# Performance work log

Measured on AMD Instinct MI355X. Metric: run time of the kernel, lower is better.

The kernel has to match this reference:

```python
import jax, jax.numpy as jnp
import numpy as np

B, N, C = 4, 4096, 64
K1, K2 = 4, 6
MLP1 = [128, 64, 64]
MLP2 = [128, 64]
EPS = 1e-5


def _sqdist(a, b):
    # a: [B,N,3], b: [B,M,3] -> [B,N,M]
    return (jnp.sum(a * a, -1)[:, :, None] + jnp.sum(b * b, -1)[:, None, :]
            - 2.0 * jnp.einsum('bnc,bmc->bnm', a, b))


def _knn_idx(k, xyz, new_xyz):
    # matches knn_point: topk of -square_distance(new_xyz, xyz)
    _, idx = jax.lax.top_k(-_sqdist(new_xyz, xyz), k)
    return idx  # [B,S,k]


def _gather(points, idx):
    # index_points: points [B,N,C], idx [B,S,K] -> [B,S,K,C]
    return jax.vmap(lambda p, i: p[i])(points, idx)


def _conv_bn_relu(x, w, g, b):
    # 1x1 Conv2d (no bias) + BatchNorm2d (train mode) + ReLU, channels-last
    y = jnp.einsum('bnkc,oc->bnko', x, w)
    m = jnp.mean(y, axis=(0, 1, 2), keepdims=True)
    v = jnp.var(y, axis=(0, 1, 2), keepdims=True)
    return jax.nn.relu((y - m) * jax.lax.rsqrt(v + EPS) * g + b)


def _quat_mul(a, b):
    # Hamilton product, matches mul_q_point ordering
    aw, ax, ay, az = a[..., 0], a[..., 1], a[..., 2], a[..., 3]
    bw, bx, by, bz = b[..., 0], b[..., 1], b[..., 2], b[..., 3]
    return jnp.stack([
        aw * bw - ax * bx - ay * by - az * bz,
        aw * bx + ax * bw + ay * bz - az * by,
        aw * by - ax * bz + ay * bw + az * bx,
        aw * bz + ax * by - ay * bx + az * bw], axis=-1)


def _inv_q(q):
    n2 = jnp.sum(q * q, -1, keepdims=True) + 1e-10
    return jnp.concatenate([q[..., :1], -q[..., 1:]], -1) / n2


def _qrot(q, v):
    # rotate points v [B,M,3] by quaternion q [B,4] via q * (0,v) * q^-1
    vq = jnp.concatenate([jnp.zeros(v.shape[:-1] + (1,), v.dtype), v], -1)
    qb = q[:, None, :]
    return _quat_mul(_quat_mul(qb, vq), _inv_q(q)[:, None, :])[..., 1:]


def setup_inputs() -> dict:
    key = jax.random.key(0)
    ks = jax.random.split(key, 32)

    def rn(i, shape, s=1.0):
        return jax.random.normal(ks[i], shape, jnp.float32) * s

    inp = {
        'pos1': rn(0, (B, N, 3)),
        'pos2': rn(1, (B, N, 3)),
        'feat1': rn(2, (B, N, C)),
        'feat2': rn(3, (B, N, C)),
        'q_coarse': rn(4, (B, 4)),
        't_coarse': rn(5, (B, 3)),
    }
    c1 = [2 * C + 3] + MLP1
    for i in range(len(MLP1)):
        inp['w1_%d' % i] = rn(6 + i, (c1[i + 1], c1[i]), 0.1)
        inp['g1_%d' % i] = jnp.ones((c1[i + 1],), jnp.float32)
        inp['b1_%d' % i] = jnp.zeros((c1[i + 1],), jnp.float32)
    c2 = [MLP1[-1] + C + 3] + MLP2
    for i in range(len(MLP2)):
        inp['w2_%d' % i] = rn(12 + i, (c2[i + 1], c2[i]), 0.1)
        inp['g2_%d' % i] = jnp.ones((c2[i + 1],), jnp.float32)
        inp['b2_%d' % i] = jnp.zeros((c2[i + 1],), jnp.float32)
    inp['wq'] = rn(20, (4, MLP2[-1]), 0.01)
    inp['bq'] = jnp.zeros((4,), jnp.float32)
    inp['wt'] = rn(21, (3, MLP2[-1]), 0.01)
    inp['bt'] = jnp.zeros((3,), jnp.float32)
    return inp


def reference(pos1, pos2, feat1, feat2, q_coarse, t_coarse,
              w1_0, g1_0, b1_0, w1_1, g1_1, b1_1, w1_2, g1_2, b1_2,
              w2_0, g2_0, b2_0, w2_1, g2_1, b2_1, wq, bq, wt, bt):
    # warp pos1 by the coarse pose (q, t)
    pos1_w = _qrot(q_coarse, pos1) + t_coarse[:, None, :]

    # cross-cloud KNN grouping (FlowEmbedding first stage)
    idx2 = _knn_idx(K2, pos2, pos1_w)                      # [B,N,K2]
    xd2 = _gather(pos2, idx2) - pos1_w[:, :, None, :]      # [B,N,K2,3]
    f2g = _gather(feat2, idx2)                             # [B,N,K2,C]
    f1r = jnp.broadcast_to(feat1[:, :, None, :], (B, N, K2, C))
    x = jnp.concatenate([xd2, f2g, f1r], -1)               # [B,N,K2,131]
    for w, g, b in ((w1_0, g1_0, b1_0), (w1_1, g1_1, b1_1), (w1_2, g1_2, b1_2)):
        x = _conv_bn_relu(x, w, g, b)
    fe = jnp.sum(x, axis=2)                                # [B,N,64] sum pool over neighbors

    # self KNN grouping (FlowEmbedding second stage)
    idx1 = _knn_idx(K1, pos1_w, pos1_w)                    # [B,N,K1]
    xd1 = _gather(pos1_w, idx1) - pos1_w[:, :, None, :]
    feg = _gather(fe, idx1)
    f1r2 = jnp.broadcast_to(feat1[:, :, None, :], (B, N, K1, C))
    x = jnp.concatenate([xd1, feg, f1r2], -1)              # [B,N,K1,131]
    for w, g, b in ((w2_0, g2_0, b2_0), (w2_1, g2_1, b2_1)):
        x = _conv_bn_relu(x, w, g, b)
    pooled = jnp.sum(jnp.sum(x, axis=2), axis=1)           # [B,64] sum pool

    # pose delta heads + quaternion composition
    q_det = pooled @ wq.T + bq
    q_det = q_det / (jnp.linalg.norm(q_det, axis=-1, keepdims=True) + 1e-10)
    t_det = pooled @ wt.T + bt
    q_new = _quat_mul(q_det, q_coarse)
    q_new = q_new / (jnp.linalg.norm(q_new, axis=-1, keepdims=True) + 1e-10)
    t_new = _qrot(q_det, t_coarse[:, None, :])[:, 0, :] + t_det
    return jnp.concatenate([q_new, t_new], -1)             # [B,7]
```

## Files before the change

kernel.cpp:

```cpp
#include <hip/hip_runtime.h>
#include <math.h>

#define B_ 4
#define N_ 4096
#define C_ 64
#define K1_ 4
#define K2_ 6
#define EPS_ 1e-5f
#define BN_ (B_ * N_)
#define NCH_ 16
#define CHP_ 256
#define STKD_ 16

typedef __attribute__((ext_vector_type(8))) short bf16x8;
typedef __attribute__((ext_vector_type(4))) float f32x4;
typedef __attribute__((ext_vector_type(2))) float f32x2;

__device__ __forceinline__ unsigned short f2bf(float f) {
  unsigned int u = __float_as_uint(f);
  unsigned int r = (u + 0x7fffu + ((u >> 16) & 1u)) >> 16;
  return (unsigned short)r;
}
__device__ __forceinline__ float bf2f(unsigned short u) {
  return __uint_as_float(((unsigned int)u) << 16);
}

template <int K>
__device__ __forceinline__ void insKi(int* kd, int k) {
  int x = k;
#pragma unroll
  for (int u = 0; u < K; ++u) {
    int lo = min(kd[u], x);
    x = max(kd[u], x);
    kd[u] = lo;
  }
}

__global__ __launch_bounds__(256) void k_init(
    const float* __restrict__ w1_0, const float* __restrict__ w1_1,
    const float* __restrict__ w1_2, const float* __restrict__ w2_0,
    const float* __restrict__ w2_1, unsigned short* __restrict__ Wf2a,
    unsigned short* __restrict__ Wf1a, unsigned short* __restrict__ Wfe,
    unsigned short* __restrict__ Wf1b, unsigned short* __restrict__ wb1,
    unsigned short* __restrict__ wb2, unsigned short* __restrict__ wb4,
    const float* __restrict__ pos1, const float* __restrict__ pos2,
    const float* __restrict__ qc, const float* __restrict__ tc,
    float4* __restrict__ pts4w, float4* __restrict__ pts4p,
    float4* __restrict__ pairW, float4* __restrict__ pairP,
    float* __restrict__ zbase) {
  int t = blockIdx.x * 256 + threadIdx.x;
  int m = blockIdx.y;
  if (m < 7) {
    switch (m) {
      case 0:
        if (t < 8192) Wf2a[t] = f2bf(w1_0[(t >> 6) * 131 + 3 + (t & 63)]);
        break;
      case 1:
        if (t < 8192) Wf1a[t] = f2bf(w1_0[(t >> 6) * 131 + 67 + (t & 63)]);
        break;
      case 2:
        if (t < 8192) Wfe[t] = f2bf(w2_0[(t >> 6) * 131 + 3 + (t & 63)]);
        break;
      case 3:
        if (t < 8192) Wf1b[t] = f2bf(w2_0[(t >> 6) * 131 + 67 + (t & 63)]);
        break;
      case 4:
        if (t < 8192) wb1[t] = f2bf(w1_1[t]);
        break;
      case 5:
        if (t < 4096) wb2[t] = f2bf(w1_2[t]);
        break;
      default:
        if (t < 8192) wb4[t] = f2bf(w2_1[t]);
        break;
    }
    return;
  }
  if (m == 8) {
    if (t < 10240) zbase[t] = 0.f;
    return;
  }
  if (t >= BN_) return;
  int b = t / N_;
  float qw = qc[b * 4 + 0], qx = qc[b * 4 + 1], qy = qc[b * 4 + 2], qz = qc[b * 4 + 3];
  float vx = pos1[t * 3 + 0], vy = pos1[t * 3 + 1], vz = pos1[t * 3 + 2];
  float aw = -(qx * vx + qy * vy + qz * vz);
  float ax = qw * vx + qy * vz - qz * vy;
  float ay = qw * vy - qx * vz + qz * vx;
  float az = qw * vz + qx * vy - qy * vx;
  float n2 = qw * qw + qx * qx + qy * qy + qz * qz + 1e-10f;
  float bw = qw / n2, bx = -qx / n2, by = -qy / n2, bz = -qz / n2;
  float rx = aw * bx + ax * bw + ay * bz - az * by;
  float ry = aw * by - ax * bz + ay * bw + az * bx;
  float rz = aw * bz + ax * by - ay * bx + az * bw;
  rx += tc[b * 3 + 0];
  ry += tc[b * 3 + 1];
  rz += tc[b * 3 + 2];
  float rw2 = rx * rx + ry * ry + rz * rz;
  pts4w[t] = make_float4(rx, ry, rz, rw2);
  int p = t >> 1, h = t & 1;
  float* bwp = (float*)&pairW[(size_t)2 * p];
  bwp[0 + h] = rx; bwp[2 + h] = ry; bwp[4 + h] = rz; bwp[6 + h] = rw2;
  float px = pos2[t * 3 + 0], py = pos2[t * 3 + 1], pz = pos2[t * 3 + 2];
  float pw2 = px * px + py * py + pz * pz;
  pts4p[t] = make_float4(px, py, pz, pw2);
  float* bpp = (float*)&pairP[(size_t)2 * p];
  bpp[0 + h] = px; bpp[2 + h] = py; bpp[4 + h] = pz; bpp[6 + h] = pw2;
}

__device__ __forceinline__ void proj_mfma_tail(const unsigned short* Xs, int tid,
                                               int row0,
                                               const unsigned short* __restrict__ Wb,
                                               float* __restrict__ dst) {
  constexpr int SP = 72;
  int l = tid & 63, wv = tid >> 6;
  int lm = l & 15, quad = l >> 4;
  int n0 = wv * 32;
  f32x4 acc[4][2];
#pragma unroll
  for (int rt = 0; rt < 4; ++rt)
#pragma unroll
    for (int ct = 0; ct < 2; ++ct) acc[rt][ct] = (f32x4)(0.f);
#pragma unroll
  for (int k0 = 0; k0 < 64; k0 += 32) {
    bf16x8 a[4], b[2];
#pragma unroll
    for (int rt = 0; rt < 4; ++rt)
      a[rt] = *(const bf16x8*)&Xs[(rt * 16 + lm) * SP + k0 + quad * 8];
#pragma unroll
    for (int ct = 0; ct < 2; ++ct)
      b[ct] = *(const bf16x8*)&Wb[(size_t)(n0 + ct * 16 + lm) * 64 + k0 + quad * 8];
#pragma unroll
    for (int rt = 0; rt < 4; ++rt)
#pragma unroll
      for (int ct = 0; ct < 2; ++ct)
        acc[rt][ct] =
            __builtin_amdgcn_mfma_f32_16x16x32_bf16(a[rt], b[ct], acc[rt][ct], 0, 0, 0);
  }
#pragma unroll
  for (int rt = 0; rt < 4; ++rt)
#pragma unroll
    for (int ct = 0; ct < 2; ++ct)
#pragma unroll
      for (int r = 0; r < 4; ++r) {
        int row = row0 + rt * 16 + quad * 4 + r;
        dst[(size_t)row * 128 + n0 + ct * 16 + lm] = acc[rt][ct][r];
      }
}

template <int K>
__device__ __forceinline__ void knn_chunk(const f32x4* __restrict__ PT, int base,
                                          float4 qv, int tid, int (*st)[256],
                                          int* __restrict__ orow) {
  f32x2 qq2 = (f32x2)(qv.w);
  f32x2 m2x = (f32x2)(-2.f * qv.x);
  f32x2 m2y = (f32x2)(-2.f * qv.y);
  f32x2 m2z = (f32x2)(-2.f * qv.z);
  int kd[K];
#pragma unroll
  for (int t = 0; t < K; ++t) kd[t] = 0x7fffffff;
  int kbd = 0x7fffffff;
  int ptr = 0;
  for (int jj = 0; jj < CHP_; jj += 4) {
    f32x4 e0 = PT[jj + 0];
    f32x4 e1 = PT[jj + 1];
    f32x4 e2 = PT[jj + 2];
    f32x4 e3 = PT[jj + 3];
    f32x2 d01 = __builtin_elementwise_fma(
        m2x, e0.xy,
        __builtin_elementwise_fma(m2y, e0.zw,
                                  __builtin_elementwise_fma(m2z, e1.xy, e1.zw + qq2)));
    f32x2 d23 = __builtin_elementwise_fma(
        m2x, e2.xy,
        __builtin_elementwise_fma(m2y, e2.zw,
                                  __builtin_elementwise_fma(m2z, e3.xy, e3.zw + qq2)));
    int j0 = base + jj;
    int k0 = (int)((__float_as_uint(d01.x) & 0xFFFFF000u) | (unsigned)(j0 + 0));
    int k1 = (int)((__float_as_uint(d01.y) & 0xFFFFF000u) | (unsigned)(j0 + 1));
    int k2 = (int)((__float_as_uint(d23.x) & 0xFFFFF000u) | (unsigned)(j0 + 2));
    int k3 = (int)((__float_as_uint(d23.y) & 0xFFFFF000u) | (unsigned)(j0 + 3));
    st[ptr][tid] = k0;
    ptr += (k0 < kbd) ? 1 : 0;
    st[ptr][tid] = k1;
    ptr += (k1 < kbd) ? 1 : 0;
    st[ptr][tid] = k2;
    ptr += (k2 < kbd) ? 1 : 0;
    st[ptr][tid] = k3;
    ptr += (k3 < kbd) ? 1 : 0;
    if (__ballot(ptr >= STKD_ - 4)) {
      for (int i = 0; i < ptr; ++i) insKi<K>(kd, st[i][tid]);
      ptr = 0;
      kbd = kd[K - 1];
    }
  }
  for (int i = 0; i < ptr; ++i) insKi<K>(kd, st[i][tid]);
#pragma unroll
  for (int t = 0; t < K; ++t) orow[t] = kd[t];
}

__global__ __launch_bounds__(256) void k_knnproj(
    const float4* __restrict__ pts4w, const float4* __restrict__ pairW,
    const float4* __restrict__ pairP, int* __restrict__ outK,
    const float* __restrict__ feat2, const unsigned short* __restrict__ Wf2a,
    float* __restrict__ P2a, const float* __restrict__ feat1,
    const unsigned short* __restrict__ Wf1a, float* __restrict__ P1a,
    const unsigned short* __restrict__ Wf1b, float* __restrict__ P1b) {
  __shared__ int st[STKD_][256];
  int tid = threadIdx.x;
  int bid = blockIdx.x;
  if (bid < 768) {
    const float* src;
    const unsigned short* Wb;
    float* dst;
    switch (bid >> 8) {
      case 0: src = feat2; Wb = Wf2a; dst = P2a; break;
      case 1: src = feat1; Wb = Wf1a; dst = P1a; break;
      default: src = feat1; Wb = Wf1b; dst = P1b; break;
    }
    unsigned short* Xs = (unsigned short*)&st[0][0];
    int row0 = (bid & 255) * 64;
    for (int e = tid; e < 64 * 16; e += 256) {
      int r = e >> 4, s = e & 15;
      float4 v = *(const float4*)&src[(size_t)(row0 + r) * 64 + s * 4];
      ushort4 o;
      o.x = f2bf(v.x); o.y = f2bf(v.y); o.z = f2bf(v.z); o.w = f2bf(v.w);
      *(ushort4*)&Xs[r * 72 + s * 4] = o;
    }
    __syncthreads();
    proj_mfma_tail(Xs, tid, row0, Wb, dst);
    return;
  }
  int kbid = bid - 768;
  int x = kbid & 15, y = (kbid >> 4) & 15, z = kbid >> 8;
  int b = z & 3;
  int which = z >> 2;
  const f32x4* __restrict__ PT =
      (const f32x4*)((which ? pairW : pairP) + (size_t)b * N_ + y * CHP_);
  int base = y * CHP_;
  int n = x * 256 + tid;
  float4 qv = pts4w[(size_t)b * N_ + n];
  int* orow = &outK[((size_t)which * BN_ * NCH_ + (size_t)(b * N_ + n) * NCH_ + y) * 6];
  if (which == 0)
    knn_chunk<6>(PT, base, qv, tid, st, orow);
  else
    knn_chunk<4>(PT, base, qv, tid, st, orow);
}

__global__ __launch_bounds__(256) void k_feproj(const unsigned short* __restrict__ y3,
                                                const float* __restrict__ stat,
                                                const float* __restrict__ g,
                                                const float* __restrict__ bb,
                                                const unsigned short* __restrict__ Wfe,
                                                float* __restrict__ Pfe) {
  constexpr int SP = 72;
  __shared__ unsigned short Xs[64 * SP];
  __shared__ float scl[C_], shf[C_];
  int tid = threadIdx.x;
  if (tid < C_) {
    int c = tid;
    float s = 0.f, s2 = 0.f;
#pragma unroll
    for (int u = 0; u < 8; ++u) {
      s += stat[c * 8 + u];
      s2 += stat[C_ * 8 + c * 8 + u];
    }
    const float invM = 1.f / (float)(BN_ * K2_);
    float m = s * invM;
    float v = s2 * invM - m * m;
    float sc = g[c] * rsqrtf(v + EPS_);
    scl[c] = sc;
    shf[c] = bb[c] - m * sc;
  }
  __syncthreads();
  int row0 = blockIdx.x * 64;
  for (int e = tid; e < 64 * 16; e += 256) {
    int r = e >> 4, s = e & 15;
    size_t base = ((size_t)(row0 + r) * K2_) * C_ + s * 4;
    float a0 = 0.f, a1 = 0.f, a2 = 0.f, a3 = 0.f;
#pragma unroll
    for (int k = 0; k < K2_; ++k) {
      ushort4 u = *(const ushort4*)&y3[base + (size_t)k * C_];
      a0 += fmaxf(fmaf(bf2f(u.x), scl[s * 4 + 0], shf[s * 4 + 0]), 0.f);
      a1 += fmaxf(fmaf(bf2f(u.y), scl[s * 4 + 1], shf[s * 4 + 1]), 0.f);
      a2 += fmaxf(fmaf(bf2f(u.z), scl[s * 4 + 2], shf[s * 4 + 2]), 0.f);
      a3 += fmaxf(fmaf(bf2f(u.w), scl[s * 4 + 3], shf[s * 4 + 3]), 0.f);
    }
    ushort4 o;
    o.x = f2bf(a0); o.y = f2bf(a1); o.z = f2bf(a2); o.w = f2bf(a3);
    *(ushort4*)&Xs[r * SP + s * 4] = o;
  }
  __syncthreads();
  proj_mfma_tail(Xs, tid, row0, Wfe, Pfe);
}

template <int KNN>
__global__ __launch_bounds__(256) void k_asm(
    const float* __restrict__ Wfull,
    const float4* __restrict__ nbrPts, const float4* __restrict__ qryPts,
    const float* __restrict__ Pj, const float* __restrict__ Pn,
    const int* __restrict__ outK,
    unsigned short* __restrict__ yout, float* __restrict__ statOut) {
  __shared__ float Wx[3][128];
  __shared__ float red[16][128];
  __shared__ int idxL[33][6];
  int tid = threadIdx.x;
  int row0 = blockIdx.x * 128;
  int first = row0 / KNN;
  int nq = (row0 + 127) / KNN - first + 1;
  if (tid < 128) {
    Wx[0][tid] = Wfull[tid * 131 + 0];
    Wx[1][tid] = Wfull[tid * 131 + 1];
    Wx[2][tid] = Wfull[tid * 131 + 2];
  }
  if (tid < nq) {
    int q = first + tid;
    int km[6];
#pragma unroll
    for (int u = 0; u < 6; ++u) km[u] = 0x7fffffff;
    size_t ib = (size_t)q * (NCH_ * 6);
    if (KNN == 6) {
      for (int c = 0; c < NCH_ * 6; ++c) insKi<6>(km, outK[ib + c]);
    } else {
      for (int ch = 0; ch < NCH_; ++ch)
#pragma unroll
        for (int u = 0; u < 4; ++u) insKi<4>(km, outK[ib + ch * 6 + u]);
    }
#pragma unroll
    for (int u = 0; u < KNN; ++u) idxL[tid][u] = km[u] & 0xFFF;
  }
  __syncthreads();
  int cg = tid & 15, rg = tid >> 4;
  int c0 = cg * 8;
  float wx0[8], wx1[8], wx2[8];
#pragma unroll
  for (int u = 0; u < 8; ++u) {
    wx0[u] = Wx[0][c0 + u];
    wx1[u] = Wx[1][c0 + u];
    wx2[u] = Wx[2][c0 + u];
  }
  float s1[8], s2[8];
#pragma unroll
  for (int u = 0; u < 8; ++u) { s1[u] = 0.f; s2[u] = 0.f; }
#pragma unroll
  for (int i = 0; i < 8; ++i) {
    int row = row0 + rg * 8 + i;
    int g = row / KNN;
    int j = idxL[g - first][row - g * KNN];
    int gj = ((g >> 12) << 12) + j;
    float4 pw = qryPts[g];
    float4 pn4 = nbrPts[gj];
    float xd0 = pn4.x - pw.x;
    float xd1 = pn4.y - pw.y;
    float xd2 = pn4.z - pw.z;
    const float* pj = &Pj[(size_t)gj * 128 + c0];
    const float* pn = &Pn[(size_t)g * 128 + c0];
    float4 a0 = *(const float4*)&pj[0];
    float4 a1 = *(const float4*)&pj[4];
    float4 b0 = *(const float4*)&pn[0];
    float4 b1 = *(const float4*)&pn[4];
    float y[8];
    y[0] = a0.x + b0.x; y[1] = a0.y + b0.y; y[2] = a0.z + b0.z; y[3] = a0.w + b0.w;
    y[4] = a1.x + b1.x; y[5] = a1.y + b1.y; y[6] = a1.z + b1.z; y[7] = a1.w + b1.w;
    ushort4 o0, o1;
    unsigned short ob[8];
#pragma unroll
    for (int u = 0; u < 8; ++u) {
      float v = y[u];
      v = fmaf(xd0, wx0[u], v);
      v = fmaf(xd1, wx1[u], v);
      v = fmaf(xd2, wx2[u], v);
      s1[u] += v;
      s2[u] = fmaf(v, v, s2[u]);
      ob[u] = f2bf(v);
    }
    o0.x = ob[0]; o0.y = ob[1]; o0.z = ob[2]; o0.w = ob[3];
    o1.x = ob[4]; o1.y = ob[5]; o1.z = ob[6]; o1.w = ob[7];
    *(ushort4*)&yout[(size_t)row * 128 + c0] = o0;
    *(ushort4*)&yout[(size_t)row * 128 + c0 + 4] = o1;
  }
  int slot = blockIdx.x & 7;
#pragma unroll
  for (int u = 0; u < 8; ++u) red[rg][c0 + u] = s1[u];
  __syncthreads();
  if (tid < 128) {
    float s = 0.f;
#pragma unroll
    for (int r = 0; r < 16; ++r) s += red[r][tid];
    atomicAdd(&statOut[tid * 8 + slot], s);
  }
  __syncthreads();
#pragma unroll
  for (int u = 0; u < 8; ++u) red[rg][c0 + u] = s2[u];
  __syncthreads();
  if (tid < 128) {
    float s = 0.f;
#pragma unroll
    for (int r = 0; r < 16; ++r) s += red[r][tid];
    atomicAdd(&statOut[128 * 8 + tid * 8 + slot], s);
  }
}

template <int CIN, int COUT, int KP>
__global__ __launch_bounds__(256) void k_layer_mfma(
    const unsigned short* __restrict__ Wb,
    const unsigned short* __restrict__ yprev,
    const float* __restrict__ statPrev, const float* __restrict__ gPrev,
    const float* __restrict__ bPrev, float prevInvM,
    unsigned short* __restrict__ yout,
    float* __restrict__ statOut) {
  constexpr int SP = KP + 8;
  constexpr int CST = COUT + 8;
  constexpr int CT = COUT / 64;
  __shared__ unsigned short Xs[64 * SP];
  __shared__ float scl[CIN];
  __shared__ float shf[CIN];

  int tid = threadIdx.x;
  int row0 = blockIdx.x * 64;

  for (int c = tid; c < CIN; c += 256) {
    float s = 0.f, s2 = 0.f;
#pragma unroll
    for (int u = 0; u < 8; ++u) {
      s += statPrev[c * 8 + u];
      s2 += statPrev[CIN * 8 + c * 8 + u];
    }
    float m = s * prevInvM;
    float v = s2 * prevInvM - m * m;
    float sc = gPrev[c] * rsqrtf(v + EPS_);
    scl[c] = sc;
    shf[c] = bPrev[c] - m * sc;
  }
  __syncthreads();
  constexpr int S8 = KP / 8;
  for (int e = tid; e < 64 * S8; e += 256) {
    int r = e / S8, s = e - r * S8;
    int row = row0 + r;
    uint4 u = *(const uint4*)&yprev[(size_t)row * CIN + s * 8];
    uint4 o;
    unsigned* up = (unsigned*)&u;
    unsigned* op = (unsigned*)&o;
#pragma unroll
    for (int w = 0; w < 4; ++w) {
      int c = s * 8 + w * 2;
      float lo = __uint_as_float(up[w] << 16);
      float hi = __uint_as_float(up[w] & 0xFFFF0000u);
      float rl = fmaxf(fmaf(lo, scl[c], shf[c]), 0.f);
      float rh = fmaxf(fmaf(hi, scl[c + 1], shf[c + 1]), 0.f);
      op[w] = (unsigned)f2bf(rl) | ((unsigned)f2bf(rh) << 16);
    }
    *(uint4*)&Xs[r * SP + s * 8] = o;
  }
  __syncthreads();

  int l = tid & 63, wv = tid >> 6;
  int lm = l & 15, quad = l >> 4;
  int n0 = wv * (COUT / 4);

  f32x4 acc[4][CT];
#pragma unroll
  for (int rt = 0; rt < 4; ++rt)
#pragma unroll
    for (int ct = 0; ct < CT; ++ct) acc[rt][ct] = (f32x4)(0.f);

#pragma unroll
  for (int k0 = 0; k0 < KP; k0 += 32) {
    bf16x8 a[4], b[CT];
#pragma unroll
    for (int rt = 0; rt < 4; ++rt)
      a[rt] = *(const bf16x8*)&Xs[(rt * 16 + lm) * SP + k0 + quad * 8];
#pragma unroll
    for (int ct = 0; ct < CT; ++ct)
      b[ct] = *(const bf16x8*)&Wb[(size_t)(n0 + ct * 16 + lm) * KP + k0 + quad * 8];
#pragma unroll
    for (int rt = 0; rt < 4; ++rt)
#pragma unroll
      for (int ct = 0; ct < CT; ++ct)
        acc[rt][ct] =
            __builtin_amdgcn_mfma_f32_16x16x32_bf16(a[rt], b[ct], acc[rt][ct], 0, 0, 0);
  }

  int slot = blockIdx.x & 7;
#pragma unroll
  for (int ct = 0; ct < CT; ++ct) {
    float s1 = 0.f, s2 = 0.f;
#pragma unroll
    for (int rt = 0; rt < 4; ++rt)
#pragma unroll
      for (int r = 0; r < 4; ++r) {
        float v = acc[rt][ct][r];
        s1 += v;
        s2 += v * v;
      }
    s1 += __shfl_xor(s1, 16);
    s1 += __shfl_xor(s1, 32);
    s2 += __shfl_xor(s2, 16);
    s2 += __shfl_xor(s2, 32);
    if (quad == 0) {
      int col = n0 + ct * 16 + lm;
      atomicAdd(&statOut[col * 8 + slot], s1);
      atomicAdd(&statOut[COUT * 8 + col * 8 + slot], s2);
    }
  }

  __syncthreads();
  unsigned short* Ys = Xs;
#pragma unroll
  for (int rt = 0; rt < 4; ++rt)
#pragma unroll
    for (int ct = 0; ct < CT; ++ct)
#pragma unroll
      for (int r = 0; r < 4; ++r)
        Ys[(rt * 16 + quad * 4 + r) * CST + n0 + ct * 16 + lm] = f2bf(acc[rt][ct][r]);
  __syncthreads();
  constexpr int SO = COUT / 8;
  for (int e = tid; e < 64 * SO; e += 256) {
    int r = e / SO, c0 = (e - r * SO) * 8;
    uint4 v = *(const uint4*)&Ys[r * CST + c0];
    *(uint4*)&yout[((size_t)(row0 + r)) * COUT + c0] = v;
  }
}

__global__ __launch_bounds__(256) void k_pooled(const unsigned short* __restrict__ y5,
                                                const float* __restrict__ stat,
                                                const float* __restrict__ g,
                                                const float* __restrict__ bb,
                                                float* __restrict__ pooled) {
  __shared__ float scl[C_], shf[C_];
  __shared__ float red[16][C_];
  if (threadIdx.x < C_) {
    int c = threadIdx.x;
    float s = 0.f, s2 = 0.f;
#pragma unroll
    for (int u = 0; u < 8; ++u) {
      s += stat[c * 8 + u];
      s2 += stat[C_ * 8 + c * 8 + u];
    }
    const float invM = 1.f / (float)(BN_ * K1_);
    float m = s * invM;
    float v = s2 * invM - m * m;
    float sc = g[c] * rsqrtf(v + EPS_);
    scl[c] = sc;
    shf[c] = bb[c] - m * sc;
  }
  __syncthreads();
  int cq = threadIdx.x & 15, rr = threadIdx.x >> 4;
  int c0 = cq * 4;
  int row0 = blockIdx.x * 64;
  int b = blockIdx.x >> 8;
  float a0 = 0.f, a1 = 0.f, a2 = 0.f, a3 = 0.f;
#pragma unroll
  for (int i = 0; i < 4; ++i) {
    int row = row0 + rr * 4 + i;
    ushort4 u = *(const ushort4*)&y5[(size_t)row * C_ + c0];
    a0 += fmaxf(fmaf(bf2f(u.x), scl[c0 + 0], shf[c0 + 0]), 0.f);
    a1 += fmaxf(fmaf(bf2f(u.y), scl[c0 + 1], shf[c0 + 1]), 0.f);
    a2 += fmaxf(fmaf(bf2f(u.z), scl[c0 + 2], shf[c0 + 2]), 0.f);
    a3 += fmaxf(fmaf(bf2f(u.w), scl[c0 + 3], shf[c0 + 3]), 0.f);
  }
  red[rr][c0 + 0] = a0;
  red[rr][c0 + 1] = a1;
  red[rr][c0 + 2] = a2;
  red[rr][c0 + 3] = a3;
  __syncthreads();
  if (threadIdx.x < C_) {
    float s = 0.f;
#pragma unroll
    for (int r = 0; r < 16; ++r) s += red[r][threadIdx.x];
    atomicAdd(&pooled[(b * C_ + threadIdx.x) * 8 + (blockIdx.x & 7)], s);
  }
}

__global__ void k_final(const float* __restrict__ pooled, const float* __restrict__ wq,
                        const float* __restrict__ bq, const float* __restrict__ wt,
                        const float* __restrict__ bt, const float* __restrict__ qc,
                        const float* __restrict__ tc, float* __restrict__ out) {
  int b = threadIdx.x;
  if (b >= B_) return;
  float P[C_];
#pragma unroll
  for (int c = 0; c < C_; ++c) {
    float s = 0.f;
#pragma unroll
    for (int u = 0; u < 8; ++u) s += pooled[(b * C_ + c) * 8 + u];
    P[c] = s;
  }
  float qd[4];
#pragma unroll
  for (int i = 0; i < 4; ++i) {
    float s = bq[i];
#pragma unroll
    for (int c = 0; c < C_; ++c) s = fmaf(P[c], wq[i * C_ + c], s);
    qd[i] = s;
  }
  float td[3];
#pragma unroll
  for (int i = 0; i < 3; ++i) {
    float s = bt[i];
#pragma unroll
    for (int c = 0; c < C_; ++c) s = fmaf(P[c], wt[i * C_ + c], s);
    td[i] = s;
  }
  float nq = sqrtf(qd[0] * qd[0] + qd[1] * qd[1] + qd[2] * qd[2] + qd[3] * qd[3]) + 1e-10f;
#pragma unroll
  for (int i = 0; i < 4; ++i) qd[i] /= nq;
  float cw = qc[b * 4 + 0], cx = qc[b * 4 + 1], cyy = qc[b * 4 + 2], cz = qc[b * 4 + 3];
  float qnw = qd[0] * cw - qd[1] * cx - qd[2] * cyy - qd[3] * cz;
  float qnx = qd[0] * cx + qd[1] * cw + qd[2] * cz - qd[3] * cyy;
  float qny = qd[0] * cyy - qd[1] * cz + qd[2] * cw + qd[3] * cx;
  float qnz = qd[0] * cz + qd[1] * cyy - qd[2] * cx + qd[3] * cw;
  float nn = sqrtf(qnw * qnw + qnx * qnx + qny * qny + qnz * qnz) + 1e-10f;
  float vx = tc[b * 3 + 0], vy = tc[b * 3 + 1], vz = tc[b * 3 + 2];
  float aw = -(qd[1] * vx + qd[2] * vy + qd[3] * vz);
  float ax = qd[0] * vx + qd[2] * vz - qd[3] * vy;
  float ay = qd[0] * vy - qd[1] * vz + qd[3] * vx;
  float az = qd[0] * vz + qd[1] * vy - qd[2] * vx;
  float n2 = qd[0] * qd[0] + qd[1] * qd[1] + qd[2] * qd[2] + qd[3] * qd[3] + 1e-10f;
  float bw = qd[0] / n2, bx = -qd[1] / n2, by = -qd[2] / n2, bz = -qd[3] / n2;
  float rx = aw * bx + ax * bw + ay * bz - az * by;
  float ry = aw * by - ax * bz + ay * bw + az * bx;
  float rz = aw * bz + ax * by - ay * bx + az * bw;
  out[b * 7 + 0] = qnw / nn;
  out[b * 7 + 1] = qnx / nn;
  out[b * 7 + 2] = qny / nn;
  out[b * 7 + 3] = qnz / nn;
  out[b * 7 + 4] = rx + td[0];
  out[b * 7 + 5] = ry + td[1];
  out[b * 7 + 6] = rz + td[2];
}

extern "C" void kernel_launch(void* const* d_in, const int* in_sizes, int n_in,
                              void* d_out, int out_size, void* d_ws, size_t ws_size,
                              hipStream_t stream) {
  const float* pos1 = (const float*)d_in[0];
  const float* pos2 = (const float*)d_in[1];
  const float* feat1 = (const float*)d_in[2];
  const float* feat2 = (const float*)d_in[3];
  const float* qc = (const float*)d_in[4];
  const float* tc = (const float*)d_in[5];
  const float* w1_0 = (const float*)d_in[6];
  const float* g1_0 = (const float*)d_in[7];
  const float* b1_0 = (const float*)d_in[8];
  const float* w1_1 = (const float*)d_in[9];
  const float* g1_1 = (const float*)d_in[10];
  const float* b1_1 = (const float*)d_in[11];
  const float* w1_2 = (const float*)d_in[12];
  const float* g1_2 = (const float*)d_in[13];
  const float* b1_2 = (const float*)d_in[14];
  const float* w2_0 = (const float*)d_in[15];
  const float* g2_0 = (const float*)d_in[16];
  const float* b2_0 = (const float*)d_in[17];
  const float* w2_1 = (const float*)d_in[18];
  const float* g2_1 = (const float*)d_in[19];
  const float* b2_1 = (const float*)d_in[20];
  const float* wq = (const float*)d_in[21];
  const float* bq = (const float*)d_in[22];
  const float* wt = (const float*)d_in[23];
  const float* bt = (const float*)d_in[24];

  float* ws = (float*)d_ws;
  const size_t off_stat = 0;
  const size_t off_pool = 8192;
  const size_t off_wb = 10240;
  const size_t off_pts4w = 36864;
  const size_t off_pts4p = 102400;
  const size_t off_pairW = 167936;
  const size_t off_pairP = 233472;
  const size_t off_knnK = 299008;
  const size_t off_P2a = 3444736;
  const size_t off_P1a = 5541888;
  const size_t off_P1b = 7639040;
  const size_t off_Pfe = 9736192;
  const size_t off_yA = 11833344;
  const size_t off_yB = 18124800;

  float* stat0 = ws + off_stat;
  float* stat1 = stat0 + 2048;
  float* stat2 = stat1 + 1024;
  float* stat3 = stat2 + 1024;
  float* stat4 = stat3 + 2048;
  float* pooled = ws + off_pool;
  unsigned short* Wf2a = (unsigned short*)(ws + off_wb);
  unsigned short* Wf1a = Wf2a + 8192;
  unsigned short* Wfe = Wf1a + 8192;
  unsigned short* Wf1b = Wfe + 8192;
  unsigned short* wb1 = Wf1b + 8192;
  unsigned short* wb2 = wb1 + 8192;
  unsigned short* wb4 = wb2 + 4096;
  float4* pts4w = (float4*)(ws + off_pts4w);
  float4* pts4p = (float4*)(ws + off_pts4p);
  float4* pairW = (float4*)(ws + off_pairW);
  float4* pairP = (float4*)(ws + off_pairP);
  int* knnK = (int*)(ws + off_knnK);
  float* P2a = ws + off_P2a;
  float* P1a = ws + off_P1a;
  float* P1b = ws + off_P1b;
  float* Pfe = ws + off_Pfe;
  unsigned short* yA = (unsigned short*)(ws + off_yA);
  unsigned short* yB = (unsigned short*)(ws + off_yB);

  k_init<<<dim3(64, 9), 256, 0, stream>>>(w1_0, w1_1, w1_2, w2_0, w2_1, Wf2a, Wf1a,
                                          Wfe, Wf1b, wb1, wb2, wb4, pos1, pos2, qc, tc,
                                          pts4w, pts4p, pairW, pairP, ws + off_stat);

  k_knnproj<<<dim3(768 + 2048), 256, 0, stream>>>(pts4w, pairW, pairP, knnK, feat2,
                                                  Wf2a, P2a, feat1, Wf1a, P1a, Wf1b,
                                                  P1b);

  k_asm<K2_><<<dim3(98304 / 128), 256, 0, stream>>>(w1_0, pts4p, pts4w, P2a, P1a, knnK,
                                                    yA, stat0);
  k_layer_mfma<128, 64, 128><<<dim3(1536), 256, 0, stream>>>(
      wb1, yA, stat0, g1_0, b1_0, 1.f / 98304.f, yB, stat1);
  k_layer_mfma<64, 64, 64><<<dim3(1536), 256, 0, stream>>>(
      wb2, yB, stat1, g1_1, b1_1, 1.f / 98304.f, yA, stat2);
  k_feproj<<<dim3(256), 256, 0, stream>>>(yA, stat2, g1_2, b1_2, Wfe, Pfe);
  k_asm<K1_><<<dim3(65536 / 128), 256, 0, stream>>>(
      w2_0, pts4w, pts4w, Pfe, P1b, knnK + (size_t)BN_ * NCH_ * 6, yA, stat3);
  k_layer_mfma<128, 64, 128><<<dim3(1024), 256, 0, stream>>>(
      wb4, yA, stat3, g2_0, b2_0, 1.f / 65536.f, yB, stat4);
  k_pooled<<<dim3(65536 / 64), 256, 0, stream>>>(yB, stat4, g2_1, b2_1, pooled);
  k_final<<<dim3(1), 64, 0, stream>>>(pooled, wq, bq, wt, bt, qc, tc, (float*)d_out);
}
```

Before: 382.0 us.

## Store projection buffers as bf16 and halve KNN chunk count with wider unroll

The per-point projection outputs (P2a, P1a, P1b, Pfe) are now written as bf16 instead of fp32 and unpacked in the assembly kernel. The intent is to halve the memory traffic of the neighbour gathers. The KNN candidate search now uses 8 chunks of 512 points instead of 16 of 256, with 8 candidates per iteration. This cuts the number of partial top-k lists to merge and the KNN block count. The cost is reduced precision in the projected features, fewer KNN blocks to occupy the GPU, and a tighter stack flush threshold.

```diff
diff --git a/kernel.cpp b/kernel.cpp
--- a/kernel.cpp
+++ b/kernel.cpp
@@ -8,8 +8,8 @@
 #define K2_ 6
 #define EPS_ 1e-5f
 #define BN_ (B_ * N_)
-#define NCH_ 16
-#define CHP_ 256
+#define NCH_ 8
+#define CHP_ 512
 #define STKD_ 16
 
 typedef __attribute__((ext_vector_type(8))) short bf16x8;
@@ -23,6 +23,14 @@
 }
 __device__ __forceinline__ float bf2f(unsigned short u) {
   return __uint_as_float(((unsigned int)u) << 16);
+}
+__device__ __forceinline__ void unpack8(uint4 u, float* f) {
+  unsigned* up = (unsigned*)&u;
+#pragma unroll
+  for (int w = 0; w < 4; ++w) {
+    f[2 * w] = __uint_as_float(up[w] << 16);
+    f[2 * w + 1] = __uint_as_float(up[w] & 0xFFFF0000u);
+  }
 }
 
 template <int K>
@@ -111,7 +119,7 @@
 __device__ __forceinline__ void proj_mfma_tail(const unsigned short* Xs, int tid,
                                                int row0,
                                                const unsigned short* __restrict__ Wb,
-                                               float* __restrict__ dst) {
+                                               unsigned short* __restrict__ dst) {
   constexpr int SP = 72;
   int l = tid & 63, wv = tid >> 6;
   int lm = l & 15, quad = l >> 4;
@@ -144,7 +152,7 @@
 #pragma unroll
       for (int r = 0; r < 4; ++r) {
         int row = row0 + rt * 16 + quad * 4 + r;
-        dst[(size_t)row * 128 + n0 + ct * 16 + lm] = acc[rt][ct][r];
+        dst[(size_t)row * 128 + n0 + ct * 16 + lm] = f2bf(acc[rt][ct][r]);
       }
 }
 
@@ -161,33 +169,34 @@
   for (int t = 0; t < K; ++t) kd[t] = 0x7fffffff;
   int kbd = 0x7fffffff;
   int ptr = 0;
-  for (int jj = 0; jj < CHP_; jj += 4) {
-    f32x4 e0 = PT[jj + 0];
-    f32x4 e1 = PT[jj + 1];
-    f32x4 e2 = PT[jj + 2];
-    f32x4 e3 = PT[jj + 3];
-    f32x2 d01 = __builtin_elementwise_fma(
-        m2x, e0.xy,
-        __builtin_elementwise_fma(m2y, e0.zw,
-                                  __builtin_elementwise_fma(m2z, e1.xy, e1.zw + qq2)));
-    f32x2 d23 = __builtin_elementwise_fma(
-        m2x, e2.xy,
-        __builtin_elementwise_fma(m2y, e2.zw,
-                                  __builtin_elementwise_fma(m2z, e3.xy, e3.zw + qq2)));
+  for (int jj = 0; jj < CHP_; jj += 8) {
+    f32x2 d[4];
+#pragma unroll
+    for (int gq = 0; gq < 2; ++gq) {
+      f32x4 e0 = PT[jj + gq * 4 + 0];
+      f32x4 e1 = PT[jj + gq * 4 + 1];
+      f32x4 e2 = PT[jj + gq * 4 + 2];
+      f32x4 e3 = PT[jj + gq * 4 + 3];
+      d[gq * 2 + 0] = __builtin_elementwise_fma(
+          m2x, e0.xy,
+          __builtin_elementwise_fma(m2y, e0.zw,
+                                    __builtin_elementwise_fma(m2z, e1.xy, e1.zw + qq2)));
+      d[gq * 2 + 1] = __builtin_elementwise_fma(
+          m2x, e2.xy,
+          __builtin_elementwise_fma(m2y, e2.zw,
+                                    __builtin_elementwise_fma(m2z, e3.xy, e3.zw + qq2)));
+    }
     int j0 = base + jj;
-    int k0 = (int)((__float_as_uint(d01.x) & 0xFFFFF000u) | (unsigned)(j0 + 0));
-    int k1 = (int)((__float_as_uint(d01.y) & 0xFFFFF000u) | (unsigned)(j0 + 1));
-    int k2 = (int)((__float_as_uint(d23.x) & 0xFFFFF000u) | (unsigned)(j0 + 2));
-    int k3 = (int)((__float_as_uint(d23.y) & 0xFFFFF000u) | (unsigned)(j0 + 3));
-    st[ptr][tid] = k0;
-    ptr += (k0 < kbd) ? 1 : 0;
-    st[ptr][tid] = k1;
-    ptr += (k1 < kbd) ? 1 : 0;
-    st[ptr][tid] = k2;
-    ptr += (k2 < kbd) ? 1 : 0;
-    st[ptr][tid] = k3;
-    ptr += (k3 < kbd) ? 1 : 0;
-    if (__ballot(ptr >= STKD_ - 4)) {
+#pragma unroll
+    for (int p = 0; p < 4; ++p) {
+      int ka = (int)((__float_as_uint(d[p].x) & 0xFFFFF000u) | (unsigned)(j0 + 2 * p));
+      int kb = (int)((__float_as_uint(d[p].y) & 0xFFFFF000u) | (unsigned)(j0 + 2 * p + 1));
+      st[ptr][tid] = ka;
+      ptr += (ka < kbd) ? 1 : 0;
+      st[ptr][tid] = kb;
+      ptr += (kb < kbd) ? 1 : 0;
+    }
+    if (__ballot(ptr >= STKD_ - 8)) {
       for (int i = 0; i < ptr; ++i) insKi<K>(kd, st[i][tid]);
       ptr = 0;
       kbd = kd[K - 1];
@@ -202,16 +211,16 @@
     const float4* __restrict__ pts4w, const float4* __restrict__ pairW,
     const float4* __restrict__ pairP, int* __restrict__ outK,
     const float* __restrict__ feat2, const unsigned short* __restrict__ Wf2a,
-    float* __restrict__ P2a, const float* __restrict__ feat1,
-    const unsigned short* __restrict__ Wf1a, float* __restrict__ P1a,
-    const unsigned short* __restrict__ Wf1b, float* __restrict__ P1b) {
+    unsigned short* __restrict__ P2a, const float* __restrict__ feat1,
+    const unsigned short* __restrict__ Wf1a, unsigned short* __restrict__ P1a,
+    const unsigned short* __restrict__ Wf1b, unsigned short* __restrict__ P1b) {
   __shared__ int st[STKD_][256];
   int tid = threadIdx.x;
   int bid = blockIdx.x;
   if (bid < 768) {
     const float* src;
     const unsigned short* Wb;
-    float* dst;
+    unsigned short* dst;
     switch (bid >> 8) {
       case 0: src = feat2; Wb = Wf2a; dst = P2a; break;
       case 1: src = feat1; Wb = Wf1a; dst = P1a; break;
@@ -231,7 +240,7 @@
     return;
   }
   int kbid = bid - 768;
-  int x = kbid & 15, y = (kbid >> 4) & 15, z = kbid >> 8;
+  int x = kbid & 15, y = (kbid >> 4) & 7, z = kbid >> 7;
   int b = z & 3;
   int which = z >> 2;
   const f32x4* __restrict__ PT =
@@ -251,7 +260,7 @@
                                                 const float* __restrict__ g,
                                                 const float* __restrict__ bb,
                                                 const unsigned short* __restrict__ Wfe,
-                                                float* __restrict__ Pfe) {
+                                                unsigned short* __restrict__ Pfe) {
   constexpr int SP = 72;
   __shared__ unsigned short Xs[64 * SP];
   __shared__ float scl[C_], shf[C_];
@@ -297,7 +306,7 @@
 __global__ __launch_bounds__(256) void k_asm(
     const float* __restrict__ Wfull,
     const float4* __restrict__ nbrPts, const float4* __restrict__ qryPts,
-    const float* __restrict__ Pj, const float* __restrict__ Pn,
+    const unsigned short* __restrict__ Pj, const unsigned short* __restrict__ Pn,
     const int* __restrict__ outK,
     unsigned short* __restrict__ yout, float* __restrict__ statOut) {
   __shared__ float Wx[3][128];
@@ -352,20 +361,16 @@
     float xd0 = pn4.x - pw.x;
     float xd1 = pn4.y - pw.y;
     float xd2 = pn4.z - pw.z;
-    const float* pj = &Pj[(size_t)gj * 128 + c0];
-    const float* pn = &Pn[(size_t)g * 128 + c0];
-    float4 a0 = *(const float4*)&pj[0];
-    float4 a1 = *(const float4*)&pj[4];
-    float4 b0 = *(const float4*)&pn[0];
-    float4 b1 = *(const float4*)&pn[4];
-    float y[8];
-    y[0] = a0.x + b0.x; y[1] = a0.y + b0.y; y[2] = a0.z + b0.z; y[3] = a0.w + b0.w;
-    y[4] = a1.x + b1.x; y[5] = a1.y + b1.y; y[6] = a1.z + b1.z; y[7] = a1.w + b1.w;
+    uint4 uj = *(const uint4*)&Pj[(size_t)gj * 128 + c0];
+    uint4 un = *(const uint4*)&Pn[(size_t)g * 128 + c0];
+    float yj[8], yn[8];
+    unpack8(uj, yj);
+    unpack8(un, yn);
     ushort4 o0, o1;
     unsigned short ob[8];
 #pragma unroll
     for (int u = 0; u < 8; ++u) {
-      float v = y[u];
+      float v = yj[u] + yn[u];
       v = fmaf(xd0, wx0[u], v);
       v = fmaf(xd1, wx1[u], v);
       v = fmaf(xd2, wx2[u], v);
@@ -667,12 +672,12 @@
   const size_t off_pairW = 167936;
   const size_t off_pairP = 233472;
   const size_t off_knnK = 299008;
-  const size_t off_P2a = 3444736;
-  const size_t off_P1a = 5541888;
-  const size_t off_P1b = 7639040;
-  const size_t off_Pfe = 9736192;
-  const size_t off_yA = 11833344;
-  const size_t off_yB = 18124800;
+  const size_t off_P2a = 1871872;
+  const size_t off_P1a = 2920448;
+  const size_t off_P1b = 3969024;
+  const size_t off_Pfe = 5017600;
+  const size_t off_yA = 6066176;
+  const size_t off_yB = 12357632;
 
   float* stat0 = ws + off_stat;
   float* stat1 = stat0 + 2048;
@@ -692,10 +697,10 @@
   float4* pairW = (float4*)(ws + off_pairW);
   float4* pairP = (float4*)(ws + off_pairP);
   int* knnK = (int*)(ws + off_knnK);
-  float* P2a = ws + off_P2a;
-  float* P1a = ws + off_P1a;
-  float* P1b = ws + off_P1b;
-  float* Pfe = ws + off_Pfe;
+  unsigned short* P2a = (unsigned short*)(ws + off_P2a);
+  unsigned short* P1a = (unsigned short*)(ws + off_P1a);
+  unsigned short* P1b = (unsigned short*)(ws + off_P1b);
+  unsigned short* Pfe = (unsigned short*)(ws + off_Pfe);
   unsigned short* yA = (unsigned short*)(ws + off_yA);
   unsigned short* yB = (unsigned short*)(ws + off_yB);
 
@@ -703,7 +708,7 @@
                                           Wfe, Wf1b, wb1, wb2, wb4, pos1, pos2, qc, tc,
                                           pts4w, pts4p, pairW, pairP, ws + off_stat);
 
-  k_knnproj<<<dim3(768 + 2048), 256, 0, stream>>>(pts4w, pairW, pairP, knnK, feat2,
+  k_knnproj<<<dim3(768 + 1024), 256, 0, stream>>>(pts4w, pairW, pairP, knnK, feat2,
                                                   Wf2a, P2a, feat1, Wf1a, P1a, Wf1b,
                                                   P1b);
 
```

Result: faster. 358.8 us (-6.1%).
